# Optimization experiments

Hardware: AMD Instinct MI355X
Metric: run time of the kernel (lower is better)

The kernel has to match this reference:

```python
import jax, jax.numpy as jnp
import numpy as np

SOS_TOKEN = 0
EOS_TOKEN = 29
B, S, ENC = 128, 400, 512   # batch, encoder max seq len, encoder feature dim
E, H, D, P, V = 256, 512, 128, 128, 30  # embed, dec hidden, dec out, attn proj, vocab
T = 600  # inference timesteps


def setup_inputs() -> dict:
    key = jax.random.key(0)
    ks = jax.random.split(key, 20)
    u = lambda k, sh: jax.random.uniform(k, sh, jnp.float32, -0.1, 0.1)
    n = lambda k, sh, s=0.02: s * jax.random.normal(k, sh, jnp.float32)
    embed = n(ks[0], (V, E), 1.0).at[EOS_TOKEN].set(0.0)  # padding_idx=EOS
    inp = dict(
        encoder_outputs=jax.random.normal(ks[1], (B, S, ENC), jnp.float32),
        encoder_lens=jax.random.randint(ks[2], (B,), S // 2, S + 1),
        embed=embed,
        W_ih1=u(ks[3], (4 * H, E + P)), W_hh1=u(ks[4], (4 * H, H)),
        b_ih1=u(ks[5], (4 * H,)), b_hh1=u(ks[6], (4 * H,)),
        W_ih2=u(ks[7], (4 * D, H)), W_hh2=u(ks[8], (4 * D, D)),
        b_ih2=u(ks[9], (4 * D,)), b_hh2=u(ks[10], (4 * D,)),
        Wk=n(ks[11], (P, ENC)), bk=jnp.zeros((P,), jnp.float32),
        Wv=n(ks[12], (P, ENC)), bv=jnp.zeros((P,), jnp.float32),
        Wq=n(ks[13], (P, D)), bq=jnp.zeros((P,), jnp.float32),
        b_char=jnp.zeros((V,), jnp.float32),
    )
    return inp


def _lstm_cell(x, h, c, W_ih, W_hh, b_ih, b_hh):
    gates = x @ W_ih.T + h @ W_hh.T + b_ih + b_hh
    i, f, g, o = jnp.split(gates, 4, axis=-1)
    c2 = jax.nn.sigmoid(f) * c + jax.nn.sigmoid(i) * jnp.tanh(g)
    return jax.nn.sigmoid(o) * jnp.tanh(c2), c2


def reference(encoder_outputs, encoder_lens, embed,
              W_ih1, W_hh1, b_ih1, b_hh1,
              W_ih2, W_hh2, b_ih2, b_hh2,
              Wk, bk, Wv, bv, Wq, bq, b_char):
    # precompute attention keys/values and mask (set_key_value_mask)
    keyv = encoder_outputs @ Wk.T + bk           # [B, S, P]
    valv = encoder_outputs @ Wv.T + bv           # [B, S, P]
    mask = jnp.arange(S)[None, :] < encoder_lens[:, None]  # [B, S]
    scale = 1.0 / np.sqrt(P).astype(np.float32)

    char0 = jnp.full((B,), SOS_TOKEN, jnp.int32)
    h1 = jnp.zeros((B, H), jnp.float32); c1 = jnp.zeros((B, H), jnp.float32)
    h2 = jnp.zeros((B, D), jnp.float32); c2 = jnp.zeros((B, D), jnp.float32)
    ctx0 = jnp.zeros((B, P), jnp.float32)

    def step(carry, _):
        char, h1, c1, h2, c2, ctx = carry
        ce = embed[char]                                   # [B, E]
        x = jnp.concatenate([ce, ctx], axis=1)
        h1n, c1n = _lstm_cell(x, h1, c1, W_ih1, W_hh1, b_ih1, b_hh1)
        h2n, c2n = _lstm_cell(h1n, h2, c2, W_ih2, W_hh2, b_ih2, b_hh2)
        q = h2n @ Wq.T + bq                                # [B, P] (attention.query)
        e = jnp.einsum('bsp,bp->bs', keyv, q) * scale
        w = jax.nn.softmax(jnp.where(mask, e, -1e9), axis=-1)
        ctxn = jnp.einsum('bs,bsp->bp', w, valv)           # [B, P]
        out_emb = jnp.concatenate([q, ctxn], axis=1)       # [B, P+P] == [B, E]
        pred = out_emb @ embed.T + b_char                  # tied char_prob weight
        charn = jnp.argmax(pred, axis=1).astype(jnp.int32)
        return (charn, h1n, c1n, h2n, c2n, ctxn), (pred, w[0])

    _, (preds, attn0) = jax.lax.scan(step, (char0, h1, c1, h2, c2, ctx0), None, length=T)
    predictions = jnp.transpose(preds, (1, 0, 2))  # [B, T, V]
    attention_plot = attn0                          # [T, S]
    return predictions, attention_plot
```

## Files before the change

kernel.cpp:

```cpp
#include <hip/hip_runtime.h>
#include <math.h>

#define B_   128
#define S_   400
#define ENC_ 512
#define E_   256
#define H_   512
#define D_   128
#define P_   128
#define V_   30
#define T_   600

#define KEYV_OFF 0
#define VALV_OFF (KEYV_OFF + B_*S_*P_)
#define H1_OFF   (VALV_OFF + B_*S_*P_)
#define C1_OFF   (H1_OFF + 2*B_*H_)
#define H2_OFF   (C1_OFF + B_*H_)
#define C2_OFF   (H2_OFF + 2*B_*D_)
#define CTX_OFF  (C2_OFF + B_*D_)
#define CHR_OFF  (CTX_OFF + B_*P_)
#define WS_FLOATS (CHR_OFF + B_)

#define PRED_N (B_*T_*V_)
#define NBLK 256
#define NTHR 512

#define W1_BASE 0
#define W2_BASE 14400
#define SCR     24704
#define LDS_FLOATS (SCR + 13056)

__device__ __forceinline__ float sigm_(float x){ return 1.0f/(1.0f + expf(-x)); }

__device__ __forceinline__ float ldA(const float* p){
  return __hip_atomic_load(p, __ATOMIC_RELAXED, __HIP_MEMORY_SCOPE_AGENT);
}
__device__ __forceinline__ void stA(float* p, float v){
  __hip_atomic_store(p, v, __ATOMIC_RELAXED, __HIP_MEMORY_SCOPE_AGENT);
}
__device__ __forceinline__ int ldAi(const int* p){
  return __hip_atomic_load(p, __ATOMIC_RELAXED, __HIP_MEMORY_SCOPE_AGENT);
}
__device__ __forceinline__ void stAi(int* p, int v){
  __hip_atomic_store(p, v, __ATOMIC_RELAXED, __HIP_MEMORY_SCOPE_AGENT);
}
__device__ __forceinline__ void ldA2f(const float* p, float& a, float& b){
  unsigned long long v = __hip_atomic_load((const unsigned long long*)p,
                         __ATOMIC_RELAXED, __HIP_MEMORY_SCOPE_AGENT);
  a = __uint_as_float((unsigned)v);
  b = __uint_as_float((unsigned)(v>>32));
}

__device__ __forceinline__ void gbar(int* bar){
  __syncthreads();
  if (threadIdx.x == 0){
    const int g0 = __hip_atomic_load(bar, __ATOMIC_RELAXED, __HIP_MEMORY_SCOPE_AGENT);
    asm volatile("" ::: "memory");
    int* leaf = bar + 64 + (blockIdx.x & 7)*32;
    int lo = __hip_atomic_fetch_add(leaf, 1, __ATOMIC_RELAXED, __HIP_MEMORY_SCOPE_AGENT);
    bool done = false;
    if (lo == 31){
      int ro = __hip_atomic_fetch_add(bar+32, 1, __ATOMIC_RELAXED, __HIP_MEMORY_SCOPE_AGENT);
      if (ro == 7){
        #pragma unroll
        for (int i=0;i<8;++i)
          __hip_atomic_store(bar+64+i*32, 0, __ATOMIC_RELAXED, __HIP_MEMORY_SCOPE_AGENT);
        __hip_atomic_store(bar+32, 0, __ATOMIC_RELAXED, __HIP_MEMORY_SCOPE_AGENT);
        asm volatile("s_waitcnt vmcnt(0)" ::: "memory");
        __hip_atomic_fetch_add(bar, 1, __ATOMIC_RELAXED, __HIP_MEMORY_SCOPE_AGENT);
        done = true;
      }
    }
    if (!done){
      while (__hip_atomic_load(bar, __ATOMIC_RELAXED, __HIP_MEMORY_SCOPE_AGENT) == g0)
        __builtin_amdgcn_s_sleep(4);
    }
  }
  __syncthreads();
}

__global__ __launch_bounds__(256) void k_kv(const float* __restrict__ enc,
    const float* __restrict__ Wk, const float* __restrict__ bk,
    const float* __restrict__ Wv, const float* __restrict__ bv,
    float* __restrict__ ws)
{
  __shared__ float As[32][68];
  __shared__ float Bs[32][68];
  const int tid = threadIdx.x;
  const int tx = tid & 15, ty = tid >> 4;
  const int n0 = blockIdx.x * 64;
  const int c0 = blockIdx.y * 64;
  float acc[4][4] = {};
  for (int k0 = 0; k0 < ENC_; k0 += 32){
    #pragma unroll
    for (int i = 0; i < 8; ++i){
      int idx = tid + 256*i;
      int kk = idx & 31, nl = idx >> 5;
      As[kk][nl] = enc[(size_t)(n0+nl)*ENC_ + k0 + kk];
    }
    #pragma unroll
    for (int i = 0; i < 8; ++i){
      int idx = tid + 256*i;
      int kk = idx & 31, cl = idx >> 5;
      int c = c0 + cl; int p = c & 127;
      const float* W = (c < 128) ? Wk : Wv;
      Bs[kk][cl] = W[(size_t)p*ENC_ + k0 + kk];
    }
    __syncthreads();
    #pragma unroll
    for (int kk = 0; kk < 32; ++kk){
      float4 a4 = *(const float4*)&As[kk][ty*4];
      float4 b4 = *(const float4*)&Bs[kk][tx*4];
      float aa[4] = {a4.x, a4.y, a4.z, a4.w};
      float bb[4] = {b4.x, b4.y, b4.z, b4.w};
      #pragma unroll
      for (int i=0;i<4;++i)
        #pragma unroll
        for (int j=0;j<4;++j) acc[i][j] += aa[i]*bb[j];
    }
    __syncthreads();
  }
  float* keyv = ws + KEYV_OFF;
  float* valv = ws + VALV_OFF;
  #pragma unroll
  for (int i=0;i<4;++i){
    int n = n0 + ty*4 + i; int b = n / S_; int s = n - b*S_;
    #pragma unroll
    for (int j=0;j<4;++j){
      int c = c0 + tx*4 + j;
      float v = acc[i][j];
      if (c < 128) keyv[((size_t)b*S_+s)*P_ + c]       = v + bk[c];
      else         valv[((size_t)b*S_+s)*P_ + (c-128)] = v + bv[c-128];
    }
  }
}

__global__ __launch_bounds__(NTHR, 1) void k_persist(
    const float* __restrict__ embed,
    const float* __restrict__ Wih1, const float* __restrict__ Whh1,
    const float* __restrict__ bih1, const float* __restrict__ bhh1,
    const float* __restrict__ Wih2, const float* __restrict__ Whh2,
    const float* __restrict__ bih2, const float* __restrict__ bhh2,
    const float* __restrict__ Wq, const float* __restrict__ bq,
    const float* __restrict__ bchar, const int* __restrict__ lens,
    float* ws, float* out)
{
  extern __shared__ float smem[];
  const int tid = threadIdx.x;
  const int bid = blockIdx.x;
  int* bar = (int*)(ws + WS_FLOATS);

  float* ctxg = ws + CTX_OFF;
  int*   chrg = (int*)(ws + CHR_OFF);

  float* Wl  = smem + W1_BASE;
  float* W2l = smem + W2_BASE;
  float* scr = smem + SCR;

  const int ib  = bid & 1;
  const int ug  = bid >> 1;
  const int b0  = ib * 64;
  const int sitem = tid >> 3;
  const int sk8   = (tid & 7) * 8;
  const int gitem = b0 + sitem;
  const int lane  = tid & 63;
  const int w8    = tid >> 6;
  const int itq   = lane & 15, rq = lane >> 4;
  const int u1    = tid >> 6;
  const int J1    = ug*4 + (u1 & 3);

  const int ig2 = bid & 3;
  const int ug2 = bid >> 2;
  const int b02 = ig2 * 32;
  const int sitem2 = tid >> 4;
  const int sk4    = (tid & 15) * 4;
  const int itemp  = tid & 15;
  const int rowp   = (tid >> 4) & 7;
  const int kw     = tid >> 7;
  const int u2     = tid >> 5;
  const int J2     = ug2*4 + (u2 & 3);

  {
    const int r = tid >> 5, c = tid & 31;
    const int R = (r >> 2)*H_ + ug*4 + (r & 3);
    #pragma unroll
    for (int j = 0; j < 7; ++j){
      int k = c*28 + j*4;
      float4 v;
      if (k < 384) v = *(const float4*)(Wih1 + (size_t)R*384 + k);
      else         v = *(const float4*)(Whh1 + (size_t)R*H_ + (k-384));
      *(float4*)&Wl[r*900 + k] = v;
    }
  }
  if (bid < 128){
    const int r = tid >> 5, c = tid & 31;
    const int R = (r >> 2)*D_ + ug2*4 + (r & 3);
    #pragma unroll
    for (int j = 0; j < 5; ++j){
      int k = c*20 + j*4;
      float4 v;
      if (k < 512) v = *(const float4*)(Wih2 + (size_t)R*H_ + k);
      else         v = *(const float4*)(Whh2 + (size_t)R*D_ + (k-512));
      *(float4*)&W2l[r*644 + k] = v;
    }
  }
  __syncthreads();

  float c1r = 0.f;
  float c2r = 0.f;
  float b1s[4], b2s[4];
  #pragma unroll
  for (int g=0; g<4; ++g){
    b1s[g] = bih1[g*H_ + J1] + bhh1[g*H_ + J1];
    b2s[g] = (bid < 128) ? (bih2[g*D_ + J2] + bhh2[g*D_ + J2]) : 0.f;
  }
  const int b3 = bid - 128;
  const float* keyv3 = ws + KEYV_OFF + (size_t)(b3 & 127)*S_*P_;
  const float* valv3 = ws + VALV_OFF + (size_t)(b3 & 127)*S_*P_;
  const int lenb = (bid >= 128) ? lens[b3] : 0;
  const float bqr  = (bid >= 128) ? bq[tid >> 2] : 0.f;
  const float bchr = (bid >= 128 && (tid >> 4) < V_) ? bchar[tid >> 4] : 0.f;

  for (int t = 0; t < T_; ++t){
    {
      const float* h1old = ws + H1_OFF + (size_t)(t&1)*B_*H_;
      float*       h1new = ws + H1_OFF + (size_t)((t+1)&1)*B_*H_;
      float* Xs  = scr;
      float* red = scr + 4352;
      const int sch = ldAi(chrg + gitem);

      float acc[4][4] = {};
      float xr[2][8];

      auto LOADX = [&](int p, float* dst){
        int kg = p*64 + sk8;
        if (kg < 256){
          const float* s = embed + (size_t)sch*E_ + kg;
          float4 a = *(const float4*)s, b = *(const float4*)(s+4);
          dst[0]=a.x; dst[1]=a.y; dst[2]=a.z; dst[3]=a.w;
          dst[4]=b.x; dst[5]=b.y; dst[6]=b.z; dst[7]=b.w;
        } else {
          const float* s = (kg < 384) ? (ctxg + (size_t)gitem*P_ + (kg-256))
                                      : (h1old + (size_t)gitem*H_ + (kg-384));
          ldA2f(s+0, dst[0], dst[1]); ldA2f(s+2, dst[2], dst[3]);
          ldA2f(s+4, dst[4], dst[5]); ldA2f(s+6, dst[6], dst[7]);
        }
      };
      LOADX(0, xr[0]); LOADX(1, xr[1]);

      for (int p = 0; p < 14; ++p){
        float* xc = xr[p & 1];
        *(float4*)&Xs[sitem*68 + sk8]     = make_float4(xc[0],xc[1],xc[2],xc[3]);
        *(float4*)&Xs[sitem*68 + sk8 + 4] = make_float4(xc[4],xc[5],xc[6],xc[7]);
        __syncthreads();
        if (p + 2 < 14) LOADX(p + 2, xr[p & 1]);
        #pragma unroll
        for (int it = 0; it < 2; ++it){
          const int kl = w8*8 + it*4;
          const int kg = p*64 + kl;
          float4 xv[4], wv[4];
          #pragma unroll
          for (int i=0;i<4;++i) xv[i] = *(const float4*)&Xs[(itq*4+i)*68 + kl];
          #pragma unroll
          for (int j=0;j<4;++j) wv[j] = *(const float4*)&Wl[(rq*4+j)*900 + kg];
          #pragma unroll
          for (int i=0;i<4;++i){
            #pragma unroll
            for (int j=0;j<4;++j){
              acc[i][j] += xv[i].x*wv[j].x + xv[i].y*wv[j].y
                         + xv[i].z*wv[j].z + xv[i].w*wv[j].w;
            }
          }
        }
        __syncthreads();
      }
      #pragma unroll
      for (int j=0;j<4;++j)
        *(float4*)&red[w8*1088 + (rq*4+j)*68 + itq*4]
          = make_float4(acc[0][j], acc[1][j], acc[2][j], acc[3][j]);
      __syncthreads();
      if (tid < 256){
        const int item = tid & 63;
        float gate[4];
        #pragma unroll
        for (int g=0; g<4; ++g){
          float s = 0.f;
          #pragma unroll
          for (int w=0; w<8; ++w) s += red[w*1088 + (g*4+(u1&3))*68 + item];
          gate[g] = s + b1s[g];
        }
        float cn = sigm_(gate[1])*c1r + sigm_(gate[0])*tanhf(gate[2]);
        float hn = sigm_(gate[3])*tanhf(cn);
        c1r = cn;
        stA(h1new + (size_t)(b0+item)*H_ + J1, hn);
      }
    }
    gbar(bar);

    if (bid < 128){
      const float* h1new = ws + H1_OFF + (size_t)((t+1)&1)*B_*H_;
      const float* h2old = ws + H2_OFF + (size_t)(t&1)*B_*D_;
      float*       h2new = ws + H2_OFF + (size_t)((t+1)&1)*B_*D_;
      float* Xs2  = scr;
      float* red2 = scr + 2176;

      float acc2[2][2] = {};
      float xr2[2][4];
      auto LOADX2 = [&](int p, float* dst){
        int kg = p*64 + sk4;
        const float* s = (kg < 512) ? (h1new + (size_t)(b02+sitem2)*H_ + kg)
                                    : (h2old + (size_t)(b02+sitem2)*D_ + (kg-512));
        ldA2f(s+0, dst[0], dst[1]); ldA2f(s+2, dst[2], dst[3]);
      };
      LOADX2(0, xr2[0]); LOADX2(1, xr2[1]);

      for (int p = 0; p < 10; ++p){
        float* xc = xr2[p & 1];
        *(float4*)&Xs2[sitem2*68 + sk4] = make_float4(xc[0],xc[1],xc[2],xc[3]);
        __syncthreads();
        if (p + 2 < 10) LOADX2(p + 2, xr2[p & 1]);
        #pragma unroll
        for (int it = 0; it < 4; ++it){
          const int kl = kw*16 + it*4;
          const int kg = p*64 + kl;
          float4 xv[2], wv[2];
          #pragma unroll
          for (int i=0;i<2;++i) xv[i] = *(const float4*)&Xs2[(itemp*2+i)*68 + kl];
          #pragma unroll
          for (int j=0;j<2;++j) wv[j] = *(const float4*)&W2l[(rowp*2+j)*644 + kg];
          #pragma unroll
          for (int i=0;i<2;++i)
            #pragma unroll
            for (int j=0;j<2;++j)
              acc2[i][j] += xv[i].x*wv[j].x + xv[i].y*wv[j].y
                          + xv[i].z*wv[j].z + xv[i].w*wv[j].w;
        }
        __syncthreads();
      }
      #pragma unroll
      for (int i=0;i<2;++i)
        #pragma unroll
        for (int j=0;j<2;++j)
          red2[kw*576 + (rowp*2+j)*36 + itemp*2+i] = acc2[i][j];
      __syncthreads();
      if (tid < 128){
        const int item = tid & 31;
        float gate[4];
        #pragma unroll
        for (int g=0; g<4; ++g){
          float s = 0.f;
          #pragma unroll
          for (int w=0; w<4; ++w) s += red2[w*576 + (g*4+(u2&3))*36 + item];
          gate[g] = s + b2s[g];
        }
        float cn = sigm_(gate[1])*c2r + sigm_(gate[0])*tanhf(gate[2]);
        float hn = sigm_(gate[3])*tanhf(cn);
        c2r = cn;
        stA(h2new + (size_t)(b02+item)*D_ + J2, hn);
      }
    }
    gbar(bar);

    if (bid >= 128){
      const float* h2new = ws + H2_OFF + (size_t)((t+1)&1)*B_*D_;
      float* hs    = scr;
      float* qs    = scr + 128;
      float* es    = scr + 256;
      float* oes   = scr + 664;
      float* preds = scr + 920;
      float* redw  = scr + 952;
      float* red3  = scr + 968;

      if (tid < 128) hs[tid] = ldA(h2new + (size_t)b3*D_ + tid);
      __syncthreads();
      {
        const int r = tid >> 2, kq = tid & 3;
        const float* wr = Wq + (size_t)r*D_ + kq*32;
        float a = 0.f;
        #pragma unroll
        for (int j=0;j<8;++j){
          float4 wv = *(const float4*)(wr + j*4);
          float4 hv = *(const float4*)&hs[kq*32 + j*4];
          a += wv.x*hv.x + wv.y*hv.y + wv.z*hv.z + wv.w*hv.w;
        }
        a += __shfl_down(a, 2, 4);
        a += __shfl_down(a, 1, 4);
        if (kq == 0) qs[r] = a + bqr;
      }
      __syncthreads();
      float sv = -INFINITY;
      if (tid < S_){
        const float4* kr = (const float4*)(keyv3 + (size_t)tid*P_);
        float a = 0.f;
        #pragma unroll 8
        for (int d=0; d<32; ++d){
          float4 kv = kr[d];
          float4 qv = *(const float4*)&qs[d*4];
          a += kv.x*qv.x + kv.y*qv.y + kv.z*qv.z + kv.w*qv.w;
        }
        sv = (tid < lenb) ? a * 0.08838834764831845f : -1e9f;
        es[tid] = sv;
      }
      float mv = sv;
      #pragma unroll
      for (int o=32; o; o>>=1) mv = fmaxf(mv, __shfl_xor(mv, o));
      if ((tid & 63) == 0) redw[tid >> 6] = mv;
      __syncthreads();
      const float m = fmaxf(fmaxf(fmaxf(redw[0],redw[1]),fmaxf(redw[2],redw[3])),
                            fmaxf(fmaxf(redw[4],redw[5]),fmaxf(redw[6],redw[7])));
      float pv = 0.f;
      if (tid < S_){ pv = expf(sv - m); es[tid] = pv; }
      float sm = pv;
      #pragma unroll
      for (int o=32; o; o>>=1) sm += __shfl_xor(sm, o);
      if ((tid & 63) == 0) redw[8 + (tid >> 6)] = sm;
      __syncthreads();
      const float sum = ((redw[8]+redw[9])+(redw[10]+redw[11]))
                      + ((redw[12]+redw[13])+(redw[14]+redw[15]));
      {
        const int p4 = tid & 31, sg = tid >> 5;
        float a0=0,a1=0,a2=0,a3=0;
        const float* vb = valv3 + (size_t)(sg*25)*P_ + p4*4;
        #pragma unroll 5
        for (int s2=0; s2<25; ++s2){
          float e = es[sg*25 + s2];
          float4 v = *(const float4*)(vb + (size_t)s2*P_);
          a0 += e*v.x; a1 += e*v.y; a2 += e*v.z; a3 += e*v.w;
        }
        *(float4*)&red3[sg*132 + p4*4] = make_float4(a0,a1,a2,a3);
      }
      __syncthreads();
      if (tid < 128){
        float c = 0.f;
        #pragma unroll
        for (int sg=0; sg<16; ++sg) c += red3[sg*132 + tid];
        c /= sum;
        stA(ctxg + (size_t)b3*P_ + tid, c);
        oes[tid] = qs[tid]; oes[128+tid] = c;
      }
      __syncthreads();
      {
        const int v = tid >> 4, k16 = tid & 15;
        float a = 0.f;
        if (v < V_){
          const float4* er = (const float4*)(embed + (size_t)v*E_ + k16*16);
          #pragma unroll
          for (int j=0;j<4;++j){
            float4 ev = er[j];
            float4 ov = *(const float4*)&oes[k16*16 + j*4];
            a += ev.x*ov.x + ev.y*ov.y + ev.z*ov.z + ev.w*ov.w;
          }
        }
        a += __shfl_down(a, 8, 16);
        a += __shfl_down(a, 4, 16);
        a += __shfl_down(a, 2, 16);
        a += __shfl_down(a, 1, 16);
        if (v < V_ && k16 == 0){
          float pvv = a + bchr;
          preds[v] = pvv;
          out[((size_t)b3*T_ + t)*V_ + v] = pvv;
        }
      }
      __syncthreads();
      if (tid < 32){
        float val = (tid < V_) ? preds[tid] : -INFINITY;
        int idx = tid;
        #pragma unroll
        for (int o = 16; o > 0; o >>= 1){
          float ov = __shfl_down(val, o, 32);
          int oi = __shfl_down(idx, o, 32);
          if (ov > val || (ov == val && oi < idx)){ val = ov; idx = oi; }
        }
        if (tid == 0) stAi(chrg + b3, idx);
      }
      if (b3 == 0 && tid < S_) out[PRED_N + (size_t)t*S_ + tid] = es[tid]/sum;
    }
    gbar(bar);
  }
}

extern "C" void kernel_launch(void* const* d_in, const int* in_sizes, int n_in,
                              void* d_out, int out_size, void* d_ws, size_t ws_size,
                              hipStream_t stream)
{
  (void)in_sizes; (void)n_in; (void)out_size; (void)ws_size;
  const float* enc   = (const float*)d_in[0];
  const int*   lens  = (const int*)d_in[1];
  const float* embed = (const float*)d_in[2];
  const float* Wih1  = (const float*)d_in[3];
  const float* Whh1  = (const float*)d_in[4];
  const float* bih1  = (const float*)d_in[5];
  const float* bhh1  = (const float*)d_in[6];
  const float* Wih2  = (const float*)d_in[7];
  const float* Whh2  = (const float*)d_in[8];
  const float* bih2  = (const float*)d_in[9];
  const float* bhh2  = (const float*)d_in[10];
  const float* Wk    = (const float*)d_in[11];
  const float* bk    = (const float*)d_in[12];
  const float* Wv    = (const float*)d_in[13];
  const float* bv    = (const float*)d_in[14];
  const float* Wq    = (const float*)d_in[15];
  const float* bq    = (const float*)d_in[16];
  const float* bchar = (const float*)d_in[17];
  float* out = (float*)d_out;
  float* ws  = (float*)d_ws;

  hipMemsetAsync((char*)d_ws + (size_t)H1_OFF*sizeof(float), 0,
                 (size_t)(WS_FLOATS - H1_OFF)*sizeof(float) + 2048, stream);
  hipLaunchKernelGGL(k_kv, dim3(800,4), dim3(256), 0, stream, enc, Wk, bk, Wv, bv, ws);

  hipFuncSetAttribute((const void*)k_persist,
                      hipFuncAttributeMaxDynamicSharedMemorySize, LDS_FLOATS*4);
  hipLaunchKernelGGL(k_persist, dim3(NBLK), dim3(NTHR), LDS_FLOATS*4, stream,
                     embed, Wih1, Whh1, bih1, bhh1,
                     Wih2, Whh2, bih2, bhh2,
                     Wq, bq, bchar, lens, ws, out);
}
```

Before: 24.94 ms.

## Transpose LSTM weight and input tiles in LDS to k-major swizzled layout

Stores both LSTM weight slices in LDS as k-major [k][16] and the per-step input tiles as k-major with an XOR-like rotation swizzle. Each wave now owns a slice of k and does rank-1 outer-product updates instead of float4 dot products. Global input loads become scalar coalesced atomic loads across k rather than 8-byte loads per item. The aim is fewer LDS bank conflicts and more coalesced global traffic, at the cost of more load instructions and a larger reduction (8 partials) in layer 2.

```diff
diff --git a/kernel.cpp b/kernel.cpp
--- a/kernel.cpp
+++ b/kernel.cpp
@@ -26,9 +26,9 @@
 #define NTHR 512
 
 #define W1_BASE 0
-#define W2_BASE 14400
-#define SCR     24704
-#define LDS_FLOATS (SCR + 13056)
+#define W2_BASE 14336
+#define SCR     24576
+#define LDS_FLOATS (SCR + 13120)
 
 __device__ __forceinline__ float sigm_(float x){ return 1.0f/(1.0f + expf(-x)); }
 
@@ -43,12 +43,6 @@
 }
 __device__ __forceinline__ void stAi(int* p, int v){
   __hip_atomic_store(p, v, __ATOMIC_RELAXED, __HIP_MEMORY_SCOPE_AGENT);
-}
-__device__ __forceinline__ void ldA2f(const float* p, float& a, float& b){
-  unsigned long long v = __hip_atomic_load((const unsigned long long*)p,
-                         __ATOMIC_RELAXED, __HIP_MEMORY_SCOPE_AGENT);
-  a = __uint_as_float((unsigned)v);
-  b = __uint_as_float((unsigned)(v>>32));
 }
 
 __device__ __forceinline__ void gbar(int* bar){
@@ -157,51 +151,42 @@
   float* W2l = smem + W2_BASE;
   float* scr = smem + SCR;
 
+  const int sk  = tid & 63;
+  const int so8 = tid >> 6;
+  const int lane = tid & 63;
+
   const int ib  = bid & 1;
   const int ug  = bid >> 1;
   const int b0  = ib * 64;
-  const int sitem = tid >> 3;
-  const int sk8   = (tid & 7) * 8;
-  const int gitem = b0 + sitem;
-  const int lane  = tid & 63;
-  const int w8    = tid >> 6;
-  const int itq   = lane & 15, rq = lane >> 4;
-  const int u1    = tid >> 6;
-  const int J1    = ug*4 + (u1 & 3);
+  const int gi8 = b0 + so8*8;
+  const int iq  = lane & 15, rq = lane >> 4;
+  const int u1  = tid >> 6;
+  const int J1  = ug*4 + (u1 & 3);
 
   const int ig2 = bid & 3;
   const int ug2 = bid >> 2;
   const int b02 = ig2 * 32;
-  const int sitem2 = tid >> 4;
-  const int sk4    = (tid & 15) * 4;
-  const int itemp  = tid & 15;
-  const int rowp   = (tid >> 4) & 7;
-  const int kw     = tid >> 7;
-  const int u2     = tid >> 5;
-  const int J2     = ug2*4 + (u2 & 3);
+  const int gi4 = b02 + so8*4;
+  const int iq2 = lane & 7, rq2 = lane >> 3;
+  const int u2  = tid >> 5;
+  const int J2  = ug2*4 + (u2 & 3);
 
   {
-    const int r = tid >> 5, c = tid & 31;
+    const int r = tid & 15, kb = tid >> 4;
     const int R = (r >> 2)*H_ + ug*4 + (r & 3);
-    #pragma unroll
-    for (int j = 0; j < 7; ++j){
-      int k = c*28 + j*4;
-      float4 v;
-      if (k < 384) v = *(const float4*)(Wih1 + (size_t)R*384 + k);
-      else         v = *(const float4*)(Whh1 + (size_t)R*H_ + (k-384));
-      *(float4*)&Wl[r*900 + k] = v;
+    for (int j = 0; j < 28; ++j){
+      int k = kb*28 + j;
+      float v = (k < 384) ? Wih1[(size_t)R*384 + k] : Whh1[(size_t)R*H_ + (k-384)];
+      Wl[k*16 + r] = v;
     }
   }
   if (bid < 128){
-    const int r = tid >> 5, c = tid & 31;
+    const int r = tid & 15, kb = tid >> 4;
     const int R = (r >> 2)*D_ + ug2*4 + (r & 3);
-    #pragma unroll
-    for (int j = 0; j < 5; ++j){
-      int k = c*20 + j*4;
-      float4 v;
-      if (k < 512) v = *(const float4*)(Wih2 + (size_t)R*H_ + k);
-      else         v = *(const float4*)(Whh2 + (size_t)R*D_ + (k-512));
-      *(float4*)&W2l[r*644 + k] = v;
+    for (int j = 0; j < 20; ++j){
+      int k = kb*20 + j;
+      float v = (k < 512) ? Wih2[(size_t)R*H_ + k] : Whh2[(size_t)R*D_ + (k-512)];
+      W2l[k*16 + r] = v;
     }
   }
   __syncthreads();
@@ -215,8 +200,9 @@
     b2s[g] = (bid < 128) ? (bih2[g*D_ + J2] + bhh2[g*D_ + J2]) : 0.f;
   }
   const int b3 = bid - 128;
-  const float* keyv3 = ws + KEYV_OFF + (size_t)(b3 & 127)*S_*P_;
-  const float* valv3 = ws + VALV_OFF + (size_t)(b3 & 127)*S_*P_;
+  const int b3i = b3 & 127;
+  const float* keyv3 = ws + KEYV_OFF + (size_t)b3i*S_*P_;
+  const float* valv3 = ws + VALV_OFF + (size_t)b3i*S_*P_;
   const int lenb = (bid >= 128) ? lens[b3] : 0;
   const float bqr  = (bid >= 128) ? bq[tid >> 2] : 0.f;
   const float bchr = (bid >= 128 && (tid >> 4) < V_) ? bchar[tid >> 4] : 0.f;
@@ -226,57 +212,59 @@
       const float* h1old = ws + H1_OFF + (size_t)(t&1)*B_*H_;
       float*       h1new = ws + H1_OFF + (size_t)((t+1)&1)*B_*H_;
       float* Xs  = scr;
-      float* red = scr + 4352;
-      const int sch = ldAi(chrg + gitem);
+      float* red = scr + 4096;
+      int*   schs= (int*)(scr + 13056);
+
+      if (tid < 64) schs[tid] = ldAi(chrg + b0 + tid);
+      __syncthreads();
+      int sch8[8];
+      #pragma unroll
+      for (int j=0;j<8;++j) sch8[j] = schs[so8*8+j];
 
       float acc[4][4] = {};
       float xr[2][8];
-
       auto LOADX = [&](int p, float* dst){
-        int kg = p*64 + sk8;
+        const int kg = p*64 + sk;
         if (kg < 256){
-          const float* s = embed + (size_t)sch*E_ + kg;
-          float4 a = *(const float4*)s, b = *(const float4*)(s+4);
-          dst[0]=a.x; dst[1]=a.y; dst[2]=a.z; dst[3]=a.w;
-          dst[4]=b.x; dst[5]=b.y; dst[6]=b.z; dst[7]=b.w;
+          #pragma unroll
+          for (int j=0;j<8;++j) dst[j] = embed[(size_t)sch8[j]*E_ + kg];
+        } else if (kg < 384){
+          #pragma unroll
+          for (int j=0;j<8;++j) dst[j] = ldA(ctxg + (size_t)(gi8+j)*P_ + (kg-256));
         } else {
-          const float* s = (kg < 384) ? (ctxg + (size_t)gitem*P_ + (kg-256))
-                                      : (h1old + (size_t)gitem*H_ + (kg-384));
-          ldA2f(s+0, dst[0], dst[1]); ldA2f(s+2, dst[2], dst[3]);
-          ldA2f(s+4, dst[4], dst[5]); ldA2f(s+6, dst[6], dst[7]);
+          #pragma unroll
+          for (int j=0;j<8;++j) dst[j] = ldA(h1old + (size_t)(gi8+j)*H_ + (kg-384));
         }
       };
       LOADX(0, xr[0]); LOADX(1, xr[1]);
 
       for (int p = 0; p < 14; ++p){
         float* xc = xr[p & 1];
-        *(float4*)&Xs[sitem*68 + sk8]     = make_float4(xc[0],xc[1],xc[2],xc[3]);
-        *(float4*)&Xs[sitem*68 + sk8 + 4] = make_float4(xc[4],xc[5],xc[6],xc[7]);
+        {
+          const int s0 = (so8*2 + sk) & 15;
+          const int s1 = (so8*2 + 1 + sk) & 15;
+          *(float4*)&Xs[sk*64 + s0*4] = make_float4(xc[0],xc[1],xc[2],xc[3]);
+          *(float4*)&Xs[sk*64 + s1*4] = make_float4(xc[4],xc[5],xc[6],xc[7]);
+        }
         __syncthreads();
         if (p + 2 < 14) LOADX(p + 2, xr[p & 1]);
         #pragma unroll
-        for (int it = 0; it < 2; ++it){
-          const int kl = w8*8 + it*4;
-          const int kg = p*64 + kl;
-          float4 xv[4], wv[4];
-          #pragma unroll
-          for (int i=0;i<4;++i) xv[i] = *(const float4*)&Xs[(itq*4+i)*68 + kl];
-          #pragma unroll
-          for (int j=0;j<4;++j) wv[j] = *(const float4*)&Wl[(rq*4+j)*900 + kg];
-          #pragma unroll
-          for (int i=0;i<4;++i){
+        for (int it = 0; it < 8; ++it){
+          const int kl = so8*8 + it;
+          float4 xv = *(const float4*)&Xs[kl*64 + ((iq + kl) & 15)*4];
+          float4 wv = *(const float4*)&Wl[(p*64 + kl)*16 + rq*4];
+          float xa[4] = {xv.x, xv.y, xv.z, xv.w};
+          float wa[4] = {wv.x, wv.y, wv.z, wv.w};
+          #pragma unroll
+          for (int i=0;i<4;++i)
             #pragma unroll
-            for (int j=0;j<4;++j){
-              acc[i][j] += xv[i].x*wv[j].x + xv[i].y*wv[j].y
-                         + xv[i].z*wv[j].z + xv[i].w*wv[j].w;
-            }
-          }
+            for (int j=0;j<4;++j) acc[i][j] += xa[i]*wa[j];
         }
         __syncthreads();
       }
       #pragma unroll
       for (int j=0;j<4;++j)
-        *(float4*)&red[w8*1088 + (rq*4+j)*68 + itq*4]
+        *(float4*)&red[so8*1088 + (rq*4+j)*68 + iq*4]
           = make_float4(acc[0][j], acc[1][j], acc[2][j], acc[3][j]);
       __syncthreads();
       if (tid < 256){
@@ -298,50 +286,49 @@
     gbar(bar);
 
     if (bid < 128){
-      const float* h1new = ws + H1_OFF + (size_t)((t+1)&1)*B_*H_;
-      const float* h2old = ws + H2_OFF + (size_t)(t&1)*B_*D_;
-      float*       h2new = ws + H2_OFF + (size_t)((t+1)&1)*B_*D_;
+      const float* h1n = ws + H1_OFF + (size_t)((t+1)&1)*B_*H_;
+      const float* h2o = ws + H2_OFF + (size_t)(t&1)*B_*D_;
+      float*       h2n = ws + H2_OFF + (size_t)((t+1)&1)*B_*D_;
       float* Xs2  = scr;
-      float* red2 = scr + 2176;
-
-      float acc2[2][2] = {};
+      float* red2 = scr + 2048;
+
+      float acc2[4][2] = {};
       float xr2[2][4];
       auto LOADX2 = [&](int p, float* dst){
-        int kg = p*64 + sk4;
-        const float* s = (kg < 512) ? (h1new + (size_t)(b02+sitem2)*H_ + kg)
-                                    : (h2old + (size_t)(b02+sitem2)*D_ + (kg-512));
-        ldA2f(s+0, dst[0], dst[1]); ldA2f(s+2, dst[2], dst[3]);
+        const int kg = p*64 + sk;
+        if (kg < 512){
+          #pragma unroll
+          for (int j=0;j<4;++j) dst[j] = ldA(h1n + (size_t)(gi4+j)*H_ + kg);
+        } else {
+          #pragma unroll
+          for (int j=0;j<4;++j) dst[j] = ldA(h2o + (size_t)(gi4+j)*D_ + (kg-512));
+        }
       };
       LOADX2(0, xr2[0]); LOADX2(1, xr2[1]);
 
       for (int p = 0; p < 10; ++p){
         float* xc = xr2[p & 1];
-        *(float4*)&Xs2[sitem2*68 + sk4] = make_float4(xc[0],xc[1],xc[2],xc[3]);
+        *(float4*)&Xs2[sk*32 + ((so8 + sk) & 7)*4] = make_float4(xc[0],xc[1],xc[2],xc[3]);
         __syncthreads();
         if (p + 2 < 10) LOADX2(p + 2, xr2[p & 1]);
         #pragma unroll
-        for (int it = 0; it < 4; ++it){
-          const int kl = kw*16 + it*4;
-          const int kg = p*64 + kl;
-          float4 xv[2], wv[2];
-          #pragma unroll
-          for (int i=0;i<2;++i) xv[i] = *(const float4*)&Xs2[(itemp*2+i)*68 + kl];
-          #pragma unroll
-          for (int j=0;j<2;++j) wv[j] = *(const float4*)&W2l[(rowp*2+j)*644 + kg];
-          #pragma unroll
-          for (int i=0;i<2;++i)
-            #pragma unroll
-            for (int j=0;j<2;++j)
-              acc2[i][j] += xv[i].x*wv[j].x + xv[i].y*wv[j].y
-                          + xv[i].z*wv[j].z + xv[i].w*wv[j].w;
+        for (int it = 0; it < 8; ++it){
+          const int kl = so8*8 + it;
+          float4 xv = *(const float4*)&Xs2[kl*32 + ((iq2 + kl) & 7)*4];
+          float2 wv = *(const float2*)&W2l[(p*64 + kl)*16 + rq2*2];
+          float xa[4] = {xv.x, xv.y, xv.z, xv.w};
+          #pragma unroll
+          for (int i=0;i<4;++i){
+            acc2[i][0] += xa[i]*wv.x;
+            acc2[i][1] += xa[i]*wv.y;
+          }
         }
         __syncthreads();
       }
       #pragma unroll
-      for (int i=0;i<2;++i)
-        #pragma unroll
-        for (int j=0;j<2;++j)
-          red2[kw*576 + (rowp*2+j)*36 + itemp*2+i] = acc2[i][j];
+      for (int j=0;j<2;++j)
+        *(float4*)&red2[so8*576 + (rq2*2+j)*36 + iq2*4]
+          = make_float4(acc2[0][j], acc2[1][j], acc2[2][j], acc2[3][j]);
       __syncthreads();
       if (tid < 128){
         const int item = tid & 31;
@@ -350,13 +337,13 @@
         for (int g=0; g<4; ++g){
           float s = 0.f;
           #pragma unroll
-          for (int w=0; w<4; ++w) s += red2[w*576 + (g*4+(u2&3))*36 + item];
+          for (int w=0; w<8; ++w) s += red2[w*576 + (g*4+(u2&3))*36 + item];
           gate[g] = s + b2s[g];
         }
         float cn = sigm_(gate[1])*c2r + sigm_(gate[0])*tanhf(gate[2]);
         float hn = sigm_(gate[3])*tanhf(cn);
         c2r = cn;
-        stA(h2new + (size_t)(b02+item)*D_ + J2, hn);
+        stA(h2n + (size_t)(b02+item)*D_ + J2, hn);
       }
     }
     gbar(bar);
```

Measured after the change: 30.61 ms. 22.7% more time.
